# Kernel tuning notes

Measured on AMD Instinct MI355X. Metric: run time of the kernel, lower is better.

## Reference

```python
import jax, jax.numpy as jnp
import numpy as np

N = 20000
E = 320000
IN_DIM = 16
H = 128
HEADS = 4
NEG_SLOPE = 0.2  # GATv2Conv default
EPS_LN = 1e-5


def setup_inputs() -> dict:
    key = jax.random.key(0)
    ks = jax.random.split(key, 16)
    f32 = jnp.float32
    def rn(k, shape, scale):
        return jax.random.normal(k, shape, dtype=f32) * scale
    s_in = 1.0 / np.sqrt(IN_DIM)
    s_h = 1.0 / np.sqrt(H)
    s_4h = 1.0 / np.sqrt(4 * H)
    s_2h = 1.0 / np.sqrt(2 * H)
    inp = {}
    inp["x"] = jax.random.normal(ks[0], (N, IN_DIM), dtype=f32)
    inp["edge_index"] = jax.random.randint(ks[1], (2, E), 0, N)
    inp["edge_attr"] = jax.random.normal(ks[2], (E, 2), dtype=f32)
    inp["emb_w"] = rn(ks[3], (IN_DIM, H), s_in)
    inp["emb_b"] = jnp.zeros((H,), f32)
    # 3 GATv2 layers stacked on leading axis
    inp["lin_l"] = rn(ks[4], (3, H, HEADS * H), s_h)
    inp["lin_r"] = rn(ks[5], (3, H, HEADS * H), s_h)
    inp["lin_edge"] = rn(ks[6], (3, 2, HEADS * H), 1.0 / np.sqrt(2.0))
    inp["att"] = rn(ks[7], (3, HEADS, H), s_h)
    inp["conv_bias01"] = jnp.zeros((2, HEADS * H), f32)  # concat=True layers
    inp["conv_bias2"] = jnp.zeros((H,), f32)             # concat=False layer
    inp["proj_w"] = rn(ks[8], (2, HEADS * H, H), s_4h)
    inp["proj_b"] = jnp.zeros((2, H), f32)
    inp["n1_g"] = jnp.ones((3, H), f32)
    inp["n1_b"] = jnp.zeros((3, H), f32)
    inp["n2_g"] = jnp.ones((3, H), f32)
    inp["n2_b"] = jnp.zeros((3, H), f32)
    inp["ffn_w1"] = rn(ks[9], (3, H, 2 * H), s_h)
    inp["ffn_b1"] = jnp.zeros((3, 2 * H), f32)
    inp["ffn_w2"] = rn(ks[10], (3, 2 * H, H), s_2h)
    inp["ffn_b2"] = jnp.zeros((3, H), f32)
    return inp


def layer_norm(x, g, b):
    mu = jnp.mean(x, axis=-1, keepdims=True)
    var = jnp.mean((x - mu) ** 2, axis=-1, keepdims=True)
    return (x - mu) * jax.lax.rsqrt(var + EPS_LN) * g + b


def gatv2(h, src, dst, eattr, Wl, Wr, We, att, bias, concat, n):
    # h: [n, H]; per-edge gather -> GATv2 attention -> segment softmax -> scatter-add
    xl = (h @ Wl).reshape(n, HEADS, H)   # source transform
    xr = (h @ Wr).reshape(n, HEADS, H)   # target transform
    ee = (eattr @ We).reshape(-1, HEADS, H)
    e = jax.nn.leaky_relu(xl[src] + xr[dst] + ee, NEG_SLOPE)  # [E', HEADS, H]
    score = jnp.einsum('ehc,hc->eh', e, att)                  # [E', HEADS]
    smax = jax.ops.segment_max(score, dst, num_segments=n)
    p = jnp.exp(score - smax[dst])
    denom = jax.ops.segment_sum(p, dst, num_segments=n)
    alpha = p / (denom[dst] + 1e-16)
    out = jax.ops.segment_sum(xl[src] * alpha[..., None], dst, num_segments=n)
    if concat:
        return out.reshape(n, HEADS * H) + bias
    return jnp.mean(out, axis=1) + bias


def reference(x, edge_index, edge_attr, emb_w, emb_b, lin_l, lin_r, lin_edge, att,
              conv_bias01, conv_bias2, proj_w, proj_b, n1_g, n1_b, n2_g, n2_b,
              ffn_w1, ffn_b1, ffn_w2, ffn_b2):
    n = x.shape[0]
    e = edge_attr.shape[0]
    # PyG add_self_loops with fill_value='mean': self-loop attr = mean of incoming edge attrs
    ones = jnp.ones((e,), x.dtype)
    deg = jax.ops.segment_sum(ones, edge_index[1], num_segments=n)
    loop_attr = jax.ops.segment_sum(edge_attr, edge_index[1], num_segments=n) / jnp.maximum(deg, 1.0)[:, None]
    ar = jnp.arange(n)
    src = jnp.concatenate([edge_index[0], ar])
    dst = jnp.concatenate([edge_index[1], ar])
    ea = jnp.concatenate([edge_attr, loop_attr], axis=0)

    h = x @ emb_w + emb_b
    for i in range(3):
        concat = i < 2
        bias = conv_bias01[i] if concat else conv_bias2
        h_in = h
        h = gatv2(h, src, dst, ea, lin_l[i], lin_r[i], lin_edge[i], att[i], bias, concat, n)
        if concat:
            h = h @ proj_w[i] + proj_b[i]
        h = layer_norm(h + h_in, n1_g[i], n1_b[i])
        h2 = h
        h = jax.nn.gelu(h @ ffn_w1[i] + ffn_b1[i], approximate=False) @ ffn_w2[i] + ffn_b2[i]
        h = layer_norm(h + h2, n2_g[i], n2_b[i])
    return h
```

## Files before the change

kernel.cpp:

```cpp
#include <hip/hip_runtime.h>
#include <math.h>

#define IN_DIM 16
#define HDIM   128
#define HEADS  4
#define HH     512
#define FFH    256
#define NEG_SLOPE 0.2f

typedef _Float16 half8 __attribute__((ext_vector_type(8)));
typedef _Float16 h8 __attribute__((ext_vector_type(8)));
typedef _Float16 h4 __attribute__((ext_vector_type(4)));
typedef _Float16 h2 __attribute__((ext_vector_type(2)));
typedef float f32x4 __attribute__((ext_vector_type(4)));
typedef int i32x4 __attribute__((ext_vector_type(4)));

struct __align__(8) Edge { int src; _Float16 ea0, ea1; };

static __device__ inline float hsum8(h8 v) {
    h4 a = __builtin_shufflevector(v, v, 0, 1, 2, 3) +
           __builtin_shufflevector(v, v, 4, 5, 6, 7);
    h2 b = __builtin_shufflevector(a, a, 0, 1) +
           __builtin_shufflevector(a, a, 2, 3);
    return (float)b[0] + (float)b[1];
}

static __device__ inline h8 shfl_xor_h8(h8 v, int off) {
    union { h8 h; i32x4 i; } u;
    u.h = v;
    u.i.x = __shfl_xor(u.i.x, off);
    u.i.y = __shfl_xor(u.i.y, off);
    u.i.z = __shfl_xor(u.i.z, off);
    u.i.w = __shfl_xor(u.i.w, off);
    return u.h;
}

struct WDesc { const float* src; _Float16* dst; int Ksrc; int lgKd; int lgN; };
struct WDescs { WDesc d[15]; };
__global__ void prep_kernel(WDescs ds,
                            const float* __restrict__ x, _Float16* __restrict__ xh, int n,
                            const float* __restrict__ we, const float* __restrict__ att,
                            const float* __restrict__ cb,
                            _Float16* __restrict__ weh, _Float16* __restrict__ atth,
                            _Float16* __restrict__ cbh) {
    int y = blockIdx.y;
    if (y < 15) {
        WDesc w = ds.d[y];
        int Kd = 1 << w.lgKd;
        int total = 1 << (w.lgKd + w.lgN);
        for (int idx = blockIdx.x * 256 + threadIdx.x; idx < total; idx += gridDim.x * 256) {
            int n2 = idx >> w.lgKd, k = idx & (Kd - 1);
            w.dst[idx] = (k < w.Ksrc) ? (_Float16)w.src[(k << w.lgN) + n2] : (_Float16)0.0f;
        }
    } else if (y == 15) {
        int total = n * 64;
        for (int idx = blockIdx.x * 256 + threadIdx.x; idx < total; idx += gridDim.x * 256) {
            int r = idx >> 6, k = idx & 63;
            xh[idx] = (k < IN_DIM) ? (_Float16)x[r * IN_DIM + k] : (_Float16)0.0f;
        }
    } else {
        int i = blockIdx.x * 256 + threadIdx.x;
        if (i < 3072) weh[i] = (_Float16)we[i];
        else if (i < 4608) atth[i - 3072] = (_Float16)att[i - 3072];
        else if (i < 5632) cbh[i - 4608] = (_Float16)cb[i - 4608];
    }
}

__global__ void deg_kernel(const int* __restrict__ ei, const float* __restrict__ eattr,
                           float* deg, float* asum, int E) {
    int e = blockIdx.x * blockDim.x + threadIdx.x;
    if (e >= E) return;
    int d = ei[E + e];
    atomicAdd(&deg[d], 1.0f);
    atomicAdd(&asum[2 * d], eattr[2 * e]);
    atomicAdd(&asum[2 * d + 1], eattr[2 * e + 1]);
}

__global__ void scan_kernel(const float* __restrict__ deg, int* row_ptr, int* cur, int n) {
    __shared__ int sums[1024];
    int tid = threadIdx.x;
    int per = (n + 1023) / 1024;
    int s0 = tid * per;
    int s1 = s0 + per; if (s1 > n) s1 = n;
    int s = 0;
    for (int i = s0; i < s1; i++) s += (int)deg[i] + 1;
    int mysum = s;
    sums[tid] = s;
    __syncthreads();
    for (int dd = 1; dd < 1024; dd <<= 1) {
        int t = (tid >= dd) ? sums[tid - dd] : 0;
        __syncthreads();
        sums[tid] += t;
        __syncthreads();
    }
    int run = sums[tid] - mysum;
    for (int i = s0; i < s1; i++) {
        row_ptr[i] = run; cur[i] = run;
        run += (int)deg[i] + 1;
    }
    if (tid == 1023) row_ptr[n] = sums[1023];
}

__global__ void scatter_kernel(const int* __restrict__ ei, const float* __restrict__ eattr,
                               const float* __restrict__ deg, const float* __restrict__ asum,
                               int* cur, Edge* csr, int E, int n) {
    int i = blockIdx.x * blockDim.x + threadIdx.x;
    if (i >= E + n) return;
    Edge ed;
    int pos;
    if (i < E) {
        int d = ei[E + i];
        pos = atomicAdd(&cur[d], 1);
        ed.src = ei[i];
        ed.ea0 = (_Float16)eattr[2 * i];
        ed.ea1 = (_Float16)eattr[2 * i + 1];
    } else {
        int nd = i - E;
        float dv = fmaxf(deg[nd], 1.0f);
        pos = atomicAdd(&cur[nd], 1);
        ed.src = nd;
        ed.ea0 = (_Float16)(asum[2 * nd] / dv);
        ed.ea1 = (_Float16)(asum[2 * nd + 1] / dv);
    }
    csr[pos] = ed;
}

template <int KT, int OUTMODE>
__global__ __launch_bounds__(256) void gemm_bstat(const _Float16* __restrict__ A, int lda,
                                                  const _Float16* __restrict__ BT,
                                                  const float* __restrict__ bias,
                                                  float* __restrict__ C32,
                                                  _Float16* __restrict__ C16,
                                                  int M, int Nstride, int numMT) {
    const int PAD = 8, KC = KT / 32;
    __shared__ _Float16 Bs[128][KT + PAD];
    int tid = threadIdx.x;
    int wave = tid >> 6, lane = tid & 63;
    int quad = lane >> 4, l16 = lane & 15;
    int wrow = (wave >> 1) * 32, wcol = (wave & 1) * 64;
    int n0 = blockIdx.x * 128;

#pragma unroll
    for (int t = 0; t < KT / 16; t++) {
        int idx = tid + t * 256;
        int r = idx / (KT / 8), kb = (idx % (KT / 8)) * 8;
        *(half8*)&Bs[r][kb] = *(const half8*)(BT + (size_t)(n0 + r) * KT + kb);
    }
    __syncthreads();

    half8 bfrag[4][KC];
#pragma unroll
    for (int j = 0; j < 4; j++)
#pragma unroll
        for (int kc = 0; kc < KC; kc++)
            bfrag[j][kc] = *(const half8*)&Bs[wcol + j * 16 + l16][kc * 32 + quad * 8];

    float biasj[4];
#pragma unroll
    for (int j = 0; j < 4; j++)
        biasj[j] = bias ? bias[n0 + wcol + j * 16 + l16] : 0.0f;

    for (int mt = blockIdx.y; mt < numMT; mt += gridDim.y) {
        int rbase = mt * 64 + wrow;
        half8 af[2][KC];
#pragma unroll
        for (int i = 0; i < 2; i++) {
            int row = rbase + i * 16 + l16;
#pragma unroll
            for (int kc = 0; kc < KC; kc++)
                af[i][kc] = (row < M) ? *(const half8*)(A + (size_t)row * lda + kc * 32 + quad * 8)
                                      : (half8)(_Float16)0.0f;
        }
        f32x4 acc[2][4] = {};
#pragma unroll
        for (int kc = 0; kc < KC; kc++)
#pragma unroll
            for (int i = 0; i < 2; i++)
#pragma unroll
                for (int j = 0; j < 4; j++)
                    acc[i][j] = __builtin_amdgcn_mfma_f32_16x16x32_f16(af[i][kc], bfrag[j][kc], acc[i][j], 0, 0, 0);
#pragma unroll
        for (int i = 0; i < 2; i++) {
#pragma unroll
            for (int r = 0; r < 4; r++) {
                int row = rbase + i * 16 + quad * 4 + r;
                if (row >= M) continue;
#pragma unroll
                for (int j = 0; j < 4; j++) {
                    int col = n0 + wcol + j * 16 + l16;
                    float v = acc[i][j][r] + biasj[j];
                    if (OUTMODE == 2) {
                        C32[(size_t)row * Nstride + col] = v;
                        C16[(size_t)row * Nstride + col] = (_Float16)v;
                    } else {
                        __builtin_nontemporal_store((_Float16)v, &C16[(size_t)row * Nstride + col]);
                    }
                }
            }
        }
    }
}

__global__ __launch_bounds__(256) void gemm_ln(const _Float16* __restrict__ A, int lda,
                                               const _Float16* __restrict__ BT,
                                               const float* __restrict__ bias,
                                               const float* __restrict__ R,
                                               const float* __restrict__ g,
                                               const float* __restrict__ b,
                                               float* __restrict__ C32,
                                               _Float16* __restrict__ C16,
                                               int M, int K) {
    const int BK = 64, PAD = 8;
    __shared__ _Float16 As[64][BK + PAD];
    __shared__ _Float16 Bs[128][BK + PAD];
    int tid = threadIdx.x;
    int wave = tid >> 6, lane = tid & 63;
    int quad = lane >> 4, l16 = lane & 15;
    int mBase = blockIdx.x * 64;

    f32x4 acc[8] = {};

    for (int k0 = 0; k0 < K; k0 += BK) {
#pragma unroll
        for (int t = 0; t < 2; t++) {
            int idx = tid + t * 256;
            int r = idx >> 3, kb = (idx & 7) * 8;
            half8 hv = {};
            int grow = mBase + r;
            if (grow < M) hv = *(const half8*)(A + (size_t)grow * lda + k0 + kb);
            *(half8*)&As[r][kb] = hv;
        }
#pragma unroll
        for (int t = 0; t < 4; t++) {
            int idx = tid + t * 256;
            int r = idx >> 3, kb = (idx & 7) * 8;
            *(half8*)&Bs[r][kb] = *(const half8*)(BT + (size_t)r * K + k0 + kb);
        }
        __syncthreads();
#pragma unroll
        for (int kc = 0; kc < 2; kc++) {
            half8 a = *(const half8*)&As[wave * 16 + l16][kc * 32 + quad * 8];
#pragma unroll
            for (int j = 0; j < 8; j++) {
                half8 bb = *(const half8*)&Bs[j * 16 + l16][kc * 32 + quad * 8];
                acc[j] = __builtin_amdgcn_mfma_f32_16x16x32_f16(a, bb, acc[j], 0, 0, 0);
            }
        }
        __syncthreads();
    }

    float gj[8], bj[8], biasj[8];
#pragma unroll
    for (int j = 0; j < 8; j++) {
        int col = j * 16 + l16;
        biasj[j] = bias[col];
        gj[j] = g[col];
        bj[j] = b[col];
    }
    int row0 = mBase + wave * 16 + quad * 4;
    float sum[4] = {}, sq[4] = {};
#pragma unroll
    for (int r = 0; r < 4; r++) {
        int row = row0 + r;
        bool ok = row < M;
        size_t base = (size_t)row * HDIM;
#pragma unroll
        for (int j = 0; j < 8; j++) {
            float v = acc[j][r] + biasj[j] + (ok ? R[base + j * 16 + l16] : 0.0f);
            acc[j][r] = v;
            sum[r] += v;
            sq[r] += v * v;
        }
    }
#pragma unroll
    for (int r = 0; r < 4; r++) {
#pragma unroll
        for (int off = 1; off < 16; off <<= 1) {
            sum[r] += __shfl_xor(sum[r], off);
            sq[r] += __shfl_xor(sq[r], off);
        }
    }
#pragma unroll
    for (int r = 0; r < 4; r++) {
        int row = row0 + r;
        if (row >= M) continue;
        size_t base = (size_t)row * HDIM;
        float mu = sum[r] * (1.0f / HDIM);
        float var = sq[r] * (1.0f / HDIM) - mu * mu;
        float invstd = rsqrtf(var + 1e-5f);
#pragma unroll
        for (int j = 0; j < 8; j++) {
            float o = (acc[j][r] - mu) * invstd * gj[j] + bj[j];
            C32[base + j * 16 + l16] = o;
            if (C16) C16[base + j * 16 + l16] = (_Float16)o;
        }
    }
}

__global__ __launch_bounds__(256) void ffn_fused(const _Float16* __restrict__ A,
                                                 const _Float16* __restrict__ W1T,
                                                 const float* __restrict__ b1,
                                                 const _Float16* __restrict__ W2T,
                                                 const float* __restrict__ b2,
                                                 const float* __restrict__ R,
                                                 const float* __restrict__ g,
                                                 const float* __restrict__ b,
                                                 float* __restrict__ C32,
                                                 _Float16* __restrict__ C16,
                                                 int M) {
    __shared__ _Float16 Ws[128][128 + 8];
    __shared__ _Float16 Mid[64][256 + 8];
    int tid = threadIdx.x;
    int wave = tid >> 6, lane = tid & 63;
    int quad = lane >> 4, l16 = lane & 15;
    int mBase = blockIdx.x * 64;

    half8 afrag[4];
    {
        int row = mBase + wave * 16 + l16;
#pragma unroll
        for (int kc = 0; kc < 4; kc++) {
            if (row < M)
                afrag[kc] = *(const half8*)(A + (size_t)row * HDIM + kc * 32 + quad * 8);
            else
                afrag[kc] = (half8)(_Float16)0.0f;
        }
    }

#pragma unroll
    for (int h = 0; h < 2; h++) {
        if (h) __syncthreads();
#pragma unroll
        for (int t = 0; t < 8; t++) {
            int idx = tid + t * 256;
            int r = idx >> 4, kb = (idx & 15) * 8;
            *(half8*)&Ws[r][kb] = *(const half8*)(W1T + (size_t)(h * 128 + r) * HDIM + kb);
        }
        __syncthreads();
        f32x4 acc[8] = {};
#pragma unroll
        for (int kc = 0; kc < 4; kc++) {
#pragma unroll
            for (int j = 0; j < 8; j++) {
                half8 bb = *(const half8*)&Ws[j * 16 + l16][kc * 32 + quad * 8];
                acc[j] = __builtin_amdgcn_mfma_f32_16x16x32_f16(afrag[kc], bb, acc[j], 0, 0, 0);
            }
        }
#pragma unroll
        for (int j = 0; j < 8; j++) {
            float bj1 = b1[h * 128 + j * 16 + l16];
#pragma unroll
            for (int r = 0; r < 4; r++) {
                float v = acc[j][r] + bj1;
                v = 0.5f * v * (1.0f + erff(v * 0.70710678118654752f));
                Mid[wave * 16 + quad * 4 + r][h * 128 + j * 16 + l16] = (_Float16)v;
            }
        }
    }
    __syncthreads();

    f32x4 acc2[8] = {};
#pragma unroll
    for (int kc2 = 0; kc2 < 2; kc2++) {
        if (kc2) __syncthreads();
#pragma unroll
        for (int t = 0; t < 8; t++) {
            int idx = tid + t * 256;
            int r = idx >> 4, kb = (idx & 15) * 8;
            *(half8*)&Ws[r][kb] = *(const half8*)(W2T + (size_t)r * FFH + kc2 * 128 + kb);
        }
        __syncthreads();
#pragma unroll
        for (int kc = 0; kc < 4; kc++) {
            half8 am = *(const half8*)&Mid[wave * 16 + l16][kc2 * 128 + kc * 32 + quad * 8];
#pragma unroll
            for (int j = 0; j < 8; j++) {
                half8 bb = *(const half8*)&Ws[j * 16 + l16][kc * 32 + quad * 8];
                acc2[j] = __builtin_amdgcn_mfma_f32_16x16x32_f16(am, bb, acc2[j], 0, 0, 0);
            }
        }
    }

    float gj[8], bj[8], b2j[8];
#pragma unroll
    for (int j = 0; j < 8; j++) {
        int col = j * 16 + l16;
        b2j[j] = b2[col];
        gj[j] = g[col];
        bj[j] = b[col];
    }
    int row0 = mBase + wave * 16 + quad * 4;
    float sum[4] = {}, sq[4] = {};
#pragma unroll
    for (int r = 0; r < 4; r++) {
        int row = row0 + r;
        bool ok = row < M;
        size_t base = (size_t)row * HDIM;
#pragma unroll
        for (int j = 0; j < 8; j++) {
            float v = acc2[j][r] + b2j[j] + (ok ? R[base + j * 16 + l16] : 0.0f);
            acc2[j][r] = v;
            sum[r] += v;
            sq[r] += v * v;
        }
    }
#pragma unroll
    for (int r = 0; r < 4; r++) {
#pragma unroll
        for (int off = 1; off < 16; off <<= 1) {
            sum[r] += __shfl_xor(sum[r], off);
            sq[r] += __shfl_xor(sq[r], off);
        }
    }
#pragma unroll
    for (int r = 0; r < 4; r++) {
        int row = row0 + r;
        if (row >= M) continue;
        size_t base = (size_t)row * HDIM;
        float mu = sum[r] * (1.0f / HDIM);
        float var = sq[r] * (1.0f / HDIM) - mu * mu;
        float invstd = rsqrtf(var + 1e-5f);
#pragma unroll
        for (int j = 0; j < 8; j++) {
            float o = (acc2[j][r] - mu) * invstd * gj[j] + bj[j];
            C32[base + j * 16 + l16] = o;
            if (C16) C16[base + j * 16 + l16] = (_Float16)o;
        }
    }
}

__global__ __launch_bounds__(256) void gat_edge_kernel(
    const _Float16* __restrict__ XLR,
    const int* __restrict__ row_ptr, const Edge* __restrict__ csr,
    const _Float16* __restrict__ WEH,
    const _Float16* __restrict__ ATTH,
    const _Float16* __restrict__ CBH,
    const float* __restrict__ cb2,
    _Float16* __restrict__ OUT16, float* __restrict__ OUT32,
    const float* __restrict__ R, const float* __restrict__ lng,
    const float* __restrict__ lnb, _Float16* __restrict__ OUT16h,
    int n, int concat) {
    int tid = threadIdx.x;
    int wave = tid >> 6, lane = tid & 63;
    int g = lane >> 5;
    int sub = lane & 31;
    int node = blockIdx.x * 4 + wave;
    if (node >= n) return;
    int c0 = sub * 16;

    h8 w0[2], w1[2], att[2], xr[2], acc[2];
#pragma unroll
    for (int k = 0; k < 2; k++) {
        w0[k]  = *(const h8*)(WEH + c0 + k * 8);
        w1[k]  = *(const h8*)(WEH + 512 + c0 + k * 8);
        att[k] = *(const h8*)(ATTH + c0 + k * 8);
        acc[k] = (h8)(_Float16)0.0f;
    }
    const _Float16 slope = (_Float16)NEG_SLOPE;

    {
        unsigned nb = ((unsigned)node << 10) + 512u + (unsigned)c0;
        xr[0] = __builtin_nontemporal_load((const h8*)(XLR + nb));
        xr[1] = __builtin_nontemporal_load((const h8*)(XLR + nb + 8));
    }

    float m = -1e30f, l = 0.0f;
    int beg = row_ptr[node], end = row_ptr[node + 1];
    int e = beg + g;

    for (; e + 2 < end; e += 4) {
        Edge eg0 = csr[e], eg1 = csr[e + 2];
        unsigned r0 = ((unsigned)eg0.src << 10) + (unsigned)c0;
        unsigned r1 = ((unsigned)eg1.src << 10) + (unsigned)c0;
        h8 x0a = *(const h8*)(XLR + r0);
        h8 x0b = *(const h8*)(XLR + r0 + 8);
        h8 x1a = *(const h8*)(XLR + r1);
        h8 x1b = *(const h8*)(XLR + r1 + 8);

        h8 v;
        h8 p80, p81;
        v = x0a + (xr[0] + w0[0] * eg0.ea0 + w1[0] * eg0.ea1);
        v = __builtin_elementwise_max(v, v * slope);
        p80 = v * att[0];
        v = x0b + (xr[1] + w0[1] * eg0.ea0 + w1[1] * eg0.ea1);
        v = __builtin_elementwise_max(v, v * slope);
        p80 += v * att[1];
        v = x1a + (xr[0] + w0[0] * eg1.ea0 + w1[0] * eg1.ea1);
        v = __builtin_elementwise_max(v, v * slope);
        p81 = v * att[0];
        v = x1b + (xr[1] + w0[1] * eg1.ea0 + w1[1] * eg1.ea1);
        v = __builtin_elementwise_max(v, v * slope);
        p81 += v * att[1];

        float p0 = hsum8(p80);
        float p1 = hsum8(p81);
        p0 += __shfl_xor(p0, 1); p1 += __shfl_xor(p1, 1);
        p0 += __shfl_xor(p0, 2); p1 += __shfl_xor(p1, 2);
        p0 += __shfl_xor(p0, 4); p1 += __shfl_xor(p1, 4);

        float mnew = fmaxf(m, fmaxf(p0, p1));
        float sc  = __expf(m - mnew);
        float e0f = __expf(p0 - mnew);
        float e1f = __expf(p1 - mnew);
        l = l * sc + e0f + e1f;
        _Float16 hs = (_Float16)sc, h0 = (_Float16)e0f, h1 = (_Float16)e1f;
        acc[0] = acc[0] * hs + x0a * h0 + x1a * h1;
        acc[1] = acc[1] * hs + x0b * h0 + x1b * h1;
        m = mnew;
    }
    for (; e < end; e += 2) {
        Edge eg0 = csr[e];
        unsigned r0 = ((unsigned)eg0.src << 10) + (unsigned)c0;
        h8 x0a = *(const h8*)(XLR + r0);
        h8 x0b = *(const h8*)(XLR + r0 + 8);
        h8 v;
        h8 p80;
        v = x0a + (xr[0] + w0[0] * eg0.ea0 + w1[0] * eg0.ea1);
        v = __builtin_elementwise_max(v, v * slope);
        p80 = v * att[0];
        v = x0b + (xr[1] + w0[1] * eg0.ea0 + w1[1] * eg0.ea1);
        v = __builtin_elementwise_max(v, v * slope);
        p80 += v * att[1];
        float p0 = hsum8(p80);
        p0 += __shfl_xor(p0, 1);
        p0 += __shfl_xor(p0, 2);
        p0 += __shfl_xor(p0, 4);
        float mnew = fmaxf(m, p0);
        float sc  = __expf(m - mnew);
        float e0f = __expf(p0 - mnew);
        l = l * sc + e0f;
        _Float16 hs = (_Float16)sc, h0 = (_Float16)e0f;
        acc[0] = acc[0] * hs + x0a * h0;
        acc[1] = acc[1] * hs + x0b * h0;
        m = mnew;
    }

    {
        float m2 = __shfl_xor(m, 32);
        float l2 = __shfl_xor(l, 32);
        h8 a20 = shfl_xor_h8(acc[0], 32);
        h8 a21 = shfl_xor_h8(acc[1], 32);
        float mS = fmaxf(m, m2);
        float sA = __expf(m - mS);
        float sB = __expf(m2 - mS);
        l = l * sA + l2 * sB;
        _Float16 hA = (_Float16)sA, hB = (_Float16)sB;
        acc[0] = acc[0] * hA + a20 * hB;
        acc[1] = acc[1] * hA + a21 * hB;
    }

    float invf = 1.0f / (l + 1e-16f);
    if (concat) {
        _Float16 hi = (_Float16)invf;
        h8 o0 = acc[0] * hi + *(const h8*)(CBH + c0);
        h8 o1 = acc[1] * hi + *(const h8*)(CBH + c0 + 8);
        if (g == 0) {
            unsigned ob = ((unsigned)node << 10) + (unsigned)c0;
            __builtin_nontemporal_store(o0, (h8*)(OUT16 + ob));
            __builtin_nontemporal_store(o1, (h8*)(OUT16 + ob + 8));
        }
    } else {
        _Float16 hi = (_Float16)invf;
        h8 t0 = acc[0] * hi;
        h8 t1 = acc[1] * hi;
        t0 = t0 + shfl_xor_h8(t0, 8);
        t1 = t1 + shfl_xor_h8(t1, 8);
        t0 = t0 + shfl_xor_h8(t0, 16);
        t1 = t1 + shfl_xor_h8(t1, 16);
        if (g == 0 && sub < 8) {
            int d0 = sub * 16;
            const float* Rp = R + (size_t)node * HDIM + d0;
            const float* cp = cb2 + d0;
            float v[16];
            float sum = 0.0f, sq = 0.0f;
#pragma unroll
            for (int q = 0; q < 4; q++) {
                f32x4 rv = *(const f32x4*)(Rp + q * 4);
                f32x4 cv = *(const f32x4*)(cp + q * 4);
#pragma unroll
                for (int t = 0; t < 4; t++) {
                    int k2 = q * 4 + t;
                    float base = (k2 < 8) ? (float)t0[k2 & 7] : (float)t1[k2 & 7];
                    float vv = base * 0.25f + cv[t] + rv[t];
                    v[k2] = vv;
                    sum += vv;
                    sq += vv * vv;
                }
            }
            sum += __shfl_xor(sum, 1); sq += __shfl_xor(sq, 1);
            sum += __shfl_xor(sum, 2); sq += __shfl_xor(sq, 2);
            sum += __shfl_xor(sum, 4); sq += __shfl_xor(sq, 4);
            float mu = sum * (1.0f / HDIM);
            float var = sq * (1.0f / HDIM) - mu * mu;
            float invstd = rsqrtf(var + 1e-5f);
            float* op = OUT32 + (size_t)node * HDIM + d0;
            _Float16* oh = OUT16h + (size_t)node * HDIM + d0;
            _Float16 o16[16];
#pragma unroll
            for (int q = 0; q < 4; q++) {
                f32x4 gv = *(const f32x4*)(lng + d0 + q * 4);
                f32x4 bv = *(const f32x4*)(lnb + d0 + q * 4);
                f32x4 ov;
#pragma unroll
                for (int t = 0; t < 4; t++) {
                    float o = (v[q * 4 + t] - mu) * invstd * gv[t] + bv[t];
                    ov[t] = o;
                    o16[q * 4 + t] = (_Float16)o;
                }
                __builtin_nontemporal_store(ov, (f32x4*)(op + q * 4));
            }
            __builtin_nontemporal_store(*(h8*)&o16[0], (h8*)(oh));
            __builtin_nontemporal_store(*(h8*)&o16[8], (h8*)(oh + 8));
        }
    }
}

extern "C" void kernel_launch(void* const* d_in, const int* in_sizes, int n_in,
                              void* d_out, int out_size, void* d_ws, size_t ws_size,
                              hipStream_t stream) {
    const float* x        = (const float*)d_in[0];
    const int*   ei       = (const int*)d_in[1];
    const float* eattr    = (const float*)d_in[2];
    const float* emb_w    = (const float*)d_in[3];
    const float* emb_b    = (const float*)d_in[4];
    const float* lin_l    = (const float*)d_in[5];
    const float* lin_r    = (const float*)d_in[6];
    const float* lin_edge = (const float*)d_in[7];
    const float* attw     = (const float*)d_in[8];
    const float* cb01     = (const float*)d_in[9];
    const float* cb2      = (const float*)d_in[10];
    const float* proj_w   = (const float*)d_in[11];
    const float* proj_b   = (const float*)d_in[12];
    const float* n1g      = (const float*)d_in[13];
    const float* n1b      = (const float*)d_in[14];
    const float* n2g      = (const float*)d_in[15];
    const float* n2b      = (const float*)d_in[16];
    const float* fw1      = (const float*)d_in[17];
    const float* fb1      = (const float*)d_in[18];
    const float* fw2      = (const float*)d_in[19];
    const float* fb2      = (const float*)d_in[20];
    float* out = (float*)d_out;

    const int n = in_sizes[0] / IN_DIM;
    const int E = in_sizes[2] / 2;
    const int EP = E + n;
    const int numMT = (n + 63) / 64;

    size_t off = 0;
    auto alloc = [&](size_t bytes) {
        void* p = (char*)d_ws + off;
        off += (bytes + 255) & ~(size_t)255;
        return p;
    };
    float* deg     = (float*)alloc((size_t)n * 4);
    float* asum    = (float*)alloc((size_t)2 * n * 4);
    int*   row_ptr = (int*)alloc((size_t)(n + 1) * 4);
    int*   cur     = (int*)alloc((size_t)n * 4);
    Edge*  csr     = (Edge*)alloc((size_t)EP * 8);
    float* H0      = (float*)alloc((size_t)n * HDIM * 4);
    float* H1      = (float*)alloc((size_t)n * HDIM * 4);
    _Float16* H0h  = (_Float16*)alloc((size_t)n * HDIM * 2);
    _Float16* H1h  = (_Float16*)alloc((size_t)n * HDIM * 2);
    _Float16* XLR  = (_Float16*)alloc((size_t)n * 1024 * 2);
    _Float16* xh   = (_Float16*)alloc((size_t)n * 64 * 2);
    _Float16* wt_emb  = (_Float16*)alloc((size_t)HDIM * 64 * 2);
    _Float16* wt_llr  = (_Float16*)alloc((size_t)3 * 1024 * HDIM * 2);
    _Float16* wt_proj = (_Float16*)alloc((size_t)2 * HDIM * HH * 2);
    _Float16* wt_f1   = (_Float16*)alloc((size_t)3 * FFH * HDIM * 2);
    _Float16* wt_f2   = (_Float16*)alloc((size_t)3 * HDIM * FFH * 2);
    _Float16* weh     = (_Float16*)alloc((size_t)3 * 1024 * 2);
    _Float16* atth    = (_Float16*)alloc((size_t)3 * 512 * 2);
    _Float16* cbh     = (_Float16*)alloc((size_t)2 * 512 * 2);
    (void)ws_size;

    WDescs ds;
    int di = 0;
    ds.d[di++] = {emb_w, wt_emb, IN_DIM, 6, 7};
    for (int i = 0; i < 3; i++) {
        ds.d[di++] = {lin_l + (size_t)i * HDIM * HH, wt_llr + (size_t)i * 1024 * HDIM, HDIM, 7, 9};
        ds.d[di++] = {lin_r + (size_t)i * HDIM * HH, wt_llr + (size_t)i * 1024 * HDIM + (size_t)512 * HDIM, HDIM, 7, 9};
    }
    for (int i = 0; i < 2; i++)
        ds.d[di++] = {proj_w + (size_t)i * HH * HDIM, wt_proj + (size_t)i * HDIM * HH, HH, 9, 7};
    for (int i = 0; i < 3; i++)
        ds.d[di++] = {fw1 + (size_t)i * HDIM * FFH, wt_f1 + (size_t)i * FFH * HDIM, HDIM, 7, 8};
    for (int i = 0; i < 3; i++)
        ds.d[di++] = {fw2 + (size_t)i * FFH * HDIM, wt_f2 + (size_t)i * HDIM * FFH, FFH, 8, 7};
    prep_kernel<<<dim3(64, 17), 256, 0, stream>>>(ds, x, xh, n,
                                                  lin_edge, attw, cb01, weh, atth, cbh);

    (void)hipMemsetAsync(deg, 0, (size_t)((char*)asum - (char*)deg) + (size_t)2 * n * 4, stream);
    deg_kernel<<<(E + 255) / 256, 256, 0, stream>>>(ei, eattr, deg, asum, E);
    scan_kernel<<<1, 1024, 0, stream>>>(deg, row_ptr, cur, n);
    scatter_kernel<<<(EP + 255) / 256, 256, 0, stream>>>(ei, eattr, deg, asum, cur, csr, E, n);

    gemm_bstat<64, 2><<<dim3(1, numMT), 256, 0, stream>>>(
        xh, 64, wt_emb, emb_b, H0, H0h, n, HDIM, numMT);

    for (int i = 0; i < 3; i++) {
        int concat = (i < 2);
        gemm_bstat<128, 1><<<dim3(8, 80), 256, 0, stream>>>(
            H0h, HDIM, wt_llr + (size_t)i * 1024 * HDIM, nullptr,
            nullptr, XLR, n, 1024, numMT);
        gat_edge_kernel<<<(n + 3) / 4, 256, 0, stream>>>(
            XLR, row_ptr, csr,
            weh + (size_t)i * 1024, atth + (size_t)i * 512,
            concat ? (cbh + (size_t)i * 512) : nullptr, cb2,
            XLR + 512, H1,
            H0, n1g + (size_t)i * HDIM, n1b + (size_t)i * HDIM, H1h,
            n, concat);
        if (concat) {
            gemm_ln<<<(n + 63) / 64, 256, 0, stream>>>(
                XLR + 512, 1024, wt_proj + (size_t)i * HDIM * HH,
                proj_b + (size_t)i * HDIM, H0,
                n1g + (size_t)i * HDIM, n1b + (size_t)i * HDIM,
                H1, H1h, n, HH);
        }
        float* lnout = (i == 2) ? out : H0;
        _Float16* lnout16 = (i == 2) ? nullptr : H0h;
        ffn_fused<<<(n + 63) / 64, 256, 0, stream>>>(
            H1h, wt_f1 + (size_t)i * FFH * HDIM, fb1 + (size_t)i * FFH,
            wt_f2 + (size_t)i * HDIM * FFH, fb2 + (size_t)i * HDIM, H1,
            n2g + (size_t)i * HDIM, n2b + (size_t)i * HDIM,
            lnout, lnout16, n);
    }
}
```

Before: 586.7 us.

## Load GEMM weights directly from global memory and drop nontemporal hints

gemm_ln and ffn_fused no longer stage A and weight tiles through shared memory with __syncthreads. Each wave now reads its MFMA fragments straight from global memory and relies on cache hits for the weights shared across blocks. Separately, the nontemporal loads and stores in the GEMM epilogue and the GAT aggregation kernel become ordinary cached accesses. This removes LDS traffic and barriers, but it adds redundant and uncoalesced global reads of the weights, and the plain stores may pollute the cache.

```diff
diff --git a/kernel.cpp b/kernel.cpp
--- a/kernel.cpp
+++ b/kernel.cpp
@@ -189,12 +189,9 @@
                 for (int j = 0; j < 4; j++) {
                     int col = n0 + wcol + j * 16 + l16;
                     float v = acc[i][j][r] + biasj[j];
-                    if (OUTMODE == 2) {
+                    if (OUTMODE == 2)
                         C32[(size_t)row * Nstride + col] = v;
-                        C16[(size_t)row * Nstride + col] = (_Float16)v;
-                    } else {
-                        __builtin_nontemporal_store((_Float16)v, &C16[(size_t)row * Nstride + col]);
-                    }
+                    C16[(size_t)row * Nstride + col] = (_Float16)v;
                 }
             }
         }
@@ -210,43 +207,21 @@
                                                float* __restrict__ C32,
                                                _Float16* __restrict__ C16,
                                                int M, int K) {
-    const int BK = 64, PAD = 8;
-    __shared__ _Float16 As[64][BK + PAD];
-    __shared__ _Float16 Bs[128][BK + PAD];
     int tid = threadIdx.x;
     int wave = tid >> 6, lane = tid & 63;
     int quad = lane >> 4, l16 = lane & 15;
     int mBase = blockIdx.x * 64;
+    int arow = mBase + wave * 16 + l16;
 
     f32x4 acc[8] = {};
-
-    for (int k0 = 0; k0 < K; k0 += BK) {
-#pragma unroll
-        for (int t = 0; t < 2; t++) {
-            int idx = tid + t * 256;
-            int r = idx >> 3, kb = (idx & 7) * 8;
-            half8 hv = {};
-            int grow = mBase + r;
-            if (grow < M) hv = *(const half8*)(A + (size_t)grow * lda + k0 + kb);
-            *(half8*)&As[r][kb] = hv;
-        }
-#pragma unroll
-        for (int t = 0; t < 4; t++) {
-            int idx = tid + t * 256;
-            int r = idx >> 3, kb = (idx & 7) * 8;
-            *(half8*)&Bs[r][kb] = *(const half8*)(BT + (size_t)r * K + k0 + kb);
-        }
-        __syncthreads();
-#pragma unroll
-        for (int kc = 0; kc < 2; kc++) {
-            half8 a = *(const half8*)&As[wave * 16 + l16][kc * 32 + quad * 8];
-#pragma unroll
-            for (int j = 0; j < 8; j++) {
-                half8 bb = *(const half8*)&Bs[j * 16 + l16][kc * 32 + quad * 8];
-                acc[j] = __builtin_amdgcn_mfma_f32_16x16x32_f16(a, bb, acc[j], 0, 0, 0);
-            }
-        }
-        __syncthreads();
+    for (int k0 = 0; k0 < K; k0 += 32) {
+        half8 a = (arow < M) ? *(const half8*)(A + (size_t)arow * lda + k0 + quad * 8)
+                             : (half8)(_Float16)0.0f;
+#pragma unroll
+        for (int j = 0; j < 8; j++) {
+            half8 bb = *(const half8*)(BT + (size_t)(j * 16 + l16) * K + k0 + quad * 8);
+            acc[j] = __builtin_amdgcn_mfma_f32_16x16x32_f16(a, bb, acc[j], 0, 0, 0);
+        }
     }
 
     float gj[8], bj[8], biasj[8];
@@ -308,7 +283,6 @@
                                                  float* __restrict__ C32,
                                                  _Float16* __restrict__ C16,
                                                  int M) {
-    __shared__ _Float16 Ws[128][128 + 8];
     __shared__ _Float16 Mid[64][256 + 8];
     int tid = threadIdx.x;
     int wave = tid >> 6, lane = tid & 63;
@@ -329,20 +303,12 @@
 
 #pragma unroll
     for (int h = 0; h < 2; h++) {
-        if (h) __syncthreads();
-#pragma unroll
-        for (int t = 0; t < 8; t++) {
-            int idx = tid + t * 256;
-            int r = idx >> 4, kb = (idx & 15) * 8;
-            *(half8*)&Ws[r][kb] = *(const half8*)(W1T + (size_t)(h * 128 + r) * HDIM + kb);
-        }
-        __syncthreads();
         f32x4 acc[8] = {};
 #pragma unroll
         for (int kc = 0; kc < 4; kc++) {
 #pragma unroll
             for (int j = 0; j < 8; j++) {
-                half8 bb = *(const half8*)&Ws[j * 16 + l16][kc * 32 + quad * 8];
+                half8 bb = *(const half8*)(W1T + (size_t)(h * 128 + j * 16 + l16) * HDIM + kc * 32 + quad * 8);
                 acc[j] = __builtin_amdgcn_mfma_f32_16x16x32_f16(afrag[kc], bb, acc[j], 0, 0, 0);
             }
         }
@@ -362,20 +328,12 @@
     f32x4 acc2[8] = {};
 #pragma unroll
     for (int kc2 = 0; kc2 < 2; kc2++) {
-        if (kc2) __syncthreads();
-#pragma unroll
-        for (int t = 0; t < 8; t++) {
-            int idx = tid + t * 256;
-            int r = idx >> 4, kb = (idx & 15) * 8;
-            *(half8*)&Ws[r][kb] = *(const half8*)(W2T + (size_t)r * FFH + kc2 * 128 + kb);
-        }
-        __syncthreads();
 #pragma unroll
         for (int kc = 0; kc < 4; kc++) {
             half8 am = *(const half8*)&Mid[wave * 16 + l16][kc2 * 128 + kc * 32 + quad * 8];
 #pragma unroll
             for (int j = 0; j < 8; j++) {
-                half8 bb = *(const half8*)&Ws[j * 16 + l16][kc * 32 + quad * 8];
+                half8 bb = *(const half8*)(W2T + (size_t)(j * 16 + l16) * FFH + kc2 * 128 + kc * 32 + quad * 8);
                 acc2[j] = __builtin_amdgcn_mfma_f32_16x16x32_f16(am, bb, acc2[j], 0, 0, 0);
             }
         }
@@ -460,8 +418,8 @@
 
     {
         unsigned nb = ((unsigned)node << 10) + 512u + (unsigned)c0;
-        xr[0] = __builtin_nontemporal_load((const h8*)(XLR + nb));
-        xr[1] = __builtin_nontemporal_load((const h8*)(XLR + nb + 8));
+        xr[0] = *(const h8*)(XLR + nb);
+        xr[1] = *(const h8*)(XLR + nb + 8);
     }
 
     float m = -1e30f, l = 0.0f;
@@ -556,8 +514,8 @@
         h8 o1 = acc[1] * hi + *(const h8*)(CBH + c0 + 8);
         if (g == 0) {
             unsigned ob = ((unsigned)node << 10) + (unsigned)c0;
-            __builtin_nontemporal_store(o0, (h8*)(OUT16 + ob));
-            __builtin_nontemporal_store(o1, (h8*)(OUT16 + ob + 8));
+            *(h8*)(OUT16 + ob) = o0;
+            *(h8*)(OUT16 + ob + 8) = o1;
         }
     } else {
         _Float16 hi = (_Float16)invf;
@@ -607,10 +565,10 @@
                     ov[t] = o;
                     o16[q * 4 + t] = (_Float16)o;
                 }
-                __builtin_nontemporal_store(ov, (f32x4*)(op + q * 4));
+                *(f32x4*)(op + q * 4) = ov;
             }
-            __builtin_nontemporal_store(*(h8*)&o16[0], (h8*)(oh));
-            __builtin_nontemporal_store(*(h8*)&o16[8], (h8*)(oh + 8));
+            *(h8*)(oh) = *(h8*)&o16[0];
+            *(h8*)(oh + 8) = *(h8*)&o16[8];
         }
     }
 }
```

Result: slower. 664.1 us (+13.2%).
